# Performance work log

Measured on AMD Instinct MI355X. Metric: run time of the kernel, lower is better.

The kernel has to match this reference:

```python
import jax, jax.numpy as jnp
import numpy as np

B, T, K = 8192, 512, 12
START_TAG, STOP_TAG = 10, 11  # '[CLS]', '[SEP]' indices in default tag_map


def setup_inputs() -> dict:
    key = jax.random.key(0)
    k1, k2 = jax.random.split(key)
    logits = jax.random.normal(k1, (B, T, K), dtype=jnp.float32)
    transitions = jax.random.normal(k2, (K, K), dtype=jnp.float32)
    # constraints applied in BiLSTMCRF.__init__
    transitions = transitions.at[:, START_TAG].set(-1000.0)
    transitions = transitions.at[STOP_TAG, :].set(-1000.0)
    return {"logits": logits, "transitions": transitions}


def reference(logits, transitions):
    """Batched Viterbi decode, matching BiLSTMCRF.__viterbi_decode.

    logits: [B, T, K] emission scores (output of hidden2tag)
    transitions: [K, K] transitions[i, j] = score of tag i -> tag j
    Returns (scores [B], paths [B, T] int32).
    """
    em = jnp.swapaxes(logits, 0, 1)  # [T, B, K]

    def step(prev, emit_t):
        # prev: [B, K] trellis at t-1; v[b, i, j] = prev[b, i] + trans[i, j]
        v = prev[:, :, None] + transitions[None, :, :]  # [B, K, K]
        best = jnp.max(v, axis=1) + emit_t              # [B, K]
        bp = jnp.argmax(v, axis=1).astype(jnp.int32)    # [B, K]
        return best, bp

    final, bps = jax.lax.scan(step, em[0], em[1:])  # final: [B,K], bps: [T-1,B,K]

    scores = jnp.max(final, axis=-1)                     # [B]
    last = jnp.argmax(final, axis=-1).astype(jnp.int32)  # [B], tag at t = T-1

    def back(nxt, bp_t):
        # bp_t[b, j] = best previous tag given tag j at the next step
        cur = jnp.take_along_axis(bp_t, nxt[:, None], axis=1)[:, 0]
        return cur, cur

    # reverse scan: processes bps[T-2] .. bps[0], outputs tags for t = 0 .. T-2
    _, rest = jax.lax.scan(back, last, bps, reverse=True)  # [T-1, B]
    paths = jnp.concatenate([rest, last[None, :]], axis=0)  # [T, B]
    return scores, jnp.swapaxes(paths, 0, 1)
```

## Files before the change

kernel.cpp:

```cpp
#include <hip/hip_runtime.h>
#include <stdint.h>


namespace {

constexpr int kB = 8192;
constexpr int kT = 512;
constexpr int kK = 12;
constexpr int kRowF = 385;

typedef float vf3 __attribute__((ext_vector_type(3)));

template <int CTRL>
__device__ __forceinline__ float dppb(float x) {
    return __int_as_float(__builtin_amdgcn_update_dpp(
        0, __float_as_int(x), CTRL, 0xf, 0xf, true));
}

__global__ __launch_bounds__(64, 1) void viterbi_fused(
    const float* __restrict__ logits,
    const float* __restrict__ trans,
    float* __restrict__ out,
    uint16_t* __restrict__ bp)
{
    __shared__ float embuf[2][16][kRowF];

    const int ln    = threadIdx.x;
    const int row   = ln >> 2;
    const int c     = ln & 3;
    const int brow0 = blockIdx.x * 16;
    const int b     = brow0 + row;
    const int j0    = 3 * c;

    float TA[12], TB[12], TC[12];
#pragma unroll
    for (int i = 0; i < 12; ++i) {
        TA[i] = trans[i * kK + j0];
        TB[i] = trans[i * kK + j0 + 1];
        TC[i] = trans[i * kK + j0 + 2];
    }

    uint16_t* __restrict__ bps = bp + (size_t)b * 511 * 4 + c;

#define DMA_CHUNK(cc) do {                                                    \
    const int dsel_ = (cc) & 1;                                               \
    _Pragma("unroll")                                                         \
    for (int r_ = 0; r_ < 16; ++r_) {                                         \
        const float* gs_ = logits + (size_t)(brow0 + r_) * (kT * kK)          \
                           + (cc) * 384 + ln;                                 \
        float* ld_ = &embuf[dsel_][r_][0];                                    \
        _Pragma("unroll")                                                     \
        for (int p_ = 0; p_ < 6; ++p_) {                                      \
            __builtin_amdgcn_global_load_lds(                                 \
                (const __attribute__((address_space(1))) void*)(gs_ + p_ * 64),\
                (__attribute__((address_space(3))) void*)(ld_ + p_ * 64),     \
                4, 0, 0);                                                     \
        }                                                                     \
    }                                                                         \
} while (0)

    auto emrd = [&](int t) -> vf3 {
        const int tc = (t < kT) ? t : (kT - 1);
        return *(const vf3*)&embuf[(tc >> 5) & 1][row][(tc & 31) * 12 + j0];
    };

    DMA_CHUNK(0);
    DMA_CHUNK(1);

    __builtin_amdgcn_wave_barrier();
    __builtin_amdgcn_s_waitcnt(0x0F70);
    __builtin_amdgcn_wave_barrier();

    vf3 iv = emrd(0);
    float n0 = iv.x, n1 = iv.y, n2 = iv.z;

    vf3 e0 = emrd(1), e1 = emrd(2), e2 = emrd(3), e3 = emrd(4);
    vf3 e4 = emrd(5), e5 = emrd(6), e6 = emrd(7), e7 = emrd(8);

#define COLX(Tc, EMITc, NOUT, BIOUT) do {                                    \
    const float x0 = p0 + Tc[0],  x1 = p1 + Tc[1],  x2 = p2 + Tc[2];         \
    const float x3 = p3 + Tc[3],  x4 = p4 + Tc[4],  x5 = p5 + Tc[5];         \
    const float x6 = p6 + Tc[6],  x7 = p7 + Tc[7],  x8 = p8 + Tc[8];         \
    const float x9 = p9 + Tc[9],  x10 = p10 + Tc[10], x11 = p11 + Tc[11];    \
    const float mA = fmaxf(fmaxf(x0, x1), x2);                               \
    const float mB = fmaxf(fmaxf(x3, x4), x5);                               \
    const float mC = fmaxf(fmaxf(x6, x7), x8);                               \
    const float mD = fmaxf(fmaxf(x9, x10), x11);                             \
    const float best = fmaxf(fmaxf(mA, mB), fmaxf(mC, mD));                  \
    int bi = 11;                                                             \
    bi = (x10 == best) ? 10 : bi;  bi = (x9 == best) ? 9 : bi;               \
    bi = (x8  == best) ?  8 : bi;  bi = (x7 == best) ? 7 : bi;               \
    bi = (x6  == best) ?  6 : bi;  bi = (x5 == best) ? 5 : bi;               \
    bi = (x4  == best) ?  4 : bi;  bi = (x3 == best) ? 3 : bi;               \
    bi = (x2  == best) ?  2 : bi;  bi = (x1 == best) ? 1 : bi;               \
    bi = (x0  == best) ?  0 : bi;                                            \
    NOUT = best + (EMITc);  BIOUT = bi;                                      \
} while (0)

#define GATHER()                                                             \
    const float p0 = dppb<0x00>(n0), p1 = dppb<0x00>(n1), p2 = dppb<0x00>(n2);\
    const float p3 = dppb<0x55>(n0), p4 = dppb<0x55>(n1), p5 = dppb<0x55>(n2);\
    const float p6 = dppb<0xAA>(n0), p7 = dppb<0xAA>(n1), p8 = dppb<0xAA>(n2);\
    const float p9 = dppb<0xFF>(n0), p10 = dppb<0xFF>(n1), p11 = dppb<0xFF>(n2)

#define STEP(TT, EV) do {                                                    \
    GATHER();                                                                \
    float q0_, q1_, q2_; int b0_, b1_, b2_;                                  \
    COLX(TA, (EV).x, q0_, b0_);                                              \
    COLX(TB, (EV).y, q1_, b1_);                                              \
    COLX(TC, (EV).z, q2_, b2_);                                              \
    n0 = q0_; n1 = q1_; n2 = q2_;                                            \
    const uint32_t w_ = (uint32_t)b0_ | ((uint32_t)b1_ << 4)                 \
                        | ((uint32_t)b2_ << 8);                              \
    bps[(size_t)((TT) - 1) * 4] = (uint16_t)w_;                              \
} while (0)

    for (int n = 0; n < 63; ++n) {
        const int tb = 8 * n + 1;

        if ((n & 3) == 2) {
            __builtin_amdgcn_wave_barrier();
            __builtin_amdgcn_s_waitcnt(0x0F70);
            __builtin_amdgcn_wave_barrier();
        }
        if ((n & 3) == 3) {
            const int cc = (n >> 2) + 2;
            if (cc <= 15) {
                __builtin_amdgcn_wave_barrier();
                __builtin_amdgcn_s_waitcnt(0xC07F);
                DMA_CHUNK(cc);
                __builtin_amdgcn_wave_barrier();
            }
        }

        const vf3 f0 = emrd(tb + 8),  f1 = emrd(tb + 9);
        const vf3 f2 = emrd(tb + 10), f3 = emrd(tb + 11);
        const vf3 f4 = emrd(tb + 12), f5 = emrd(tb + 13);
        const vf3 f6 = emrd(tb + 14), f7 = emrd(tb + 15);

        STEP(tb + 0, e0); STEP(tb + 1, e1); STEP(tb + 2, e2); STEP(tb + 3, e3);
        STEP(tb + 4, e4); STEP(tb + 5, e5); STEP(tb + 6, e6); STEP(tb + 7, e7);

        e0 = f0; e1 = f1; e2 = f2; e3 = f3;
        e4 = f4; e5 = f5; e6 = f6; e7 = f7;
    }

    STEP(505, e0); STEP(506, e1); STEP(507, e2); STEP(508, e3);
    STEP(509, e4); STEP(510, e5); STEP(511, e6);

#undef STEP
#undef DMA_CHUNK

    float best;
    int last;
    {
        GATHER();
        const float mA = fmaxf(fmaxf(p0, p1), p2);
        const float mB = fmaxf(fmaxf(p3, p4), p5);
        const float mC = fmaxf(fmaxf(p6, p7), p8);
        const float mD = fmaxf(fmaxf(p9, p10), p11);
        best = fmaxf(fmaxf(mA, mB), fmaxf(mC, mD));
        int bi = 11;
        bi = (p10 == best) ? 10 : bi;  bi = (p9 == best) ? 9 : bi;
        bi = (p8  == best) ?  8 : bi;  bi = (p7 == best) ? 7 : bi;
        bi = (p6  == best) ?  6 : bi;  bi = (p5 == best) ? 5 : bi;
        bi = (p4  == best) ?  4 : bi;  bi = (p3 == best) ? 3 : bi;
        bi = (p2  == best) ?  2 : bi;  bi = (p1 == best) ? 1 : bi;
        bi = (p0  == best) ?  0 : bi;
        last = bi;
    }
#undef GATHER
#undef COLX

    __syncthreads();

    if (c == 0) {
        out[b] = best;
        float* __restrict__ paths = out + kB + (size_t)b * kT;
        paths[kT - 1] = (float)last;

        int tag = last;
        const uint2* __restrict__ rec = (const uint2*)(bp + (size_t)b * 511 * 4);
#pragma unroll 4
        for (int s = 510; s >= 0; --s) {
            const uint2 q = rec[s];
            const int d3 = (tag * 11) >> 5;
            const int rm = tag - 3 * d3;
            const uint32_t dw = (d3 & 2) ? q.y : q.x;
            const int sh = ((d3 & 1) << 4) + (rm << 2);
            tag = (int)((dw >> sh) & 0xF);
            paths[s] = (float)tag;
        }
    }
}

}

extern "C" void kernel_launch(void* const* d_in, const int* in_sizes, int n_in,
                              void* d_out, int out_size, void* d_ws, size_t ws_size,
                              hipStream_t stream) {
    const float* logits = (const float*)d_in[0];
    const float* trans  = (const float*)d_in[1];
    float* out = (float*)d_out;
    uint16_t* bp = (uint16_t*)d_ws;

    const int threads = 64;
    const int blocks = kB / 16;
    viterbi_fused<<<blocks, threads, 0, stream>>>(logits, trans, out, bp);
}
```

Baseline: 496.0 us.

## Map one lane per tag with 4 rows per wave and packed backpointers

```diff
diff --git a/kernel.cpp b/kernel.cpp
--- a/kernel.cpp
+++ b/kernel.cpp
@@ -7,45 +7,43 @@
 constexpr int kB = 8192;
 constexpr int kT = 512;
 constexpr int kK = 12;
-constexpr int kRowF = 385;
-
-typedef float vf3 __attribute__((ext_vector_type(3)));
-
-template <int CTRL>
-__device__ __forceinline__ float dppb(float x) {
-    return __int_as_float(__builtin_amdgcn_update_dpp(
-        0, __float_as_int(x), CTRL, 0xf, 0xf, true));
-}
-
-__global__ __launch_bounds__(64, 1) void viterbi_fused(
+constexpr int kRows = 4;
+constexpr int kRowF = 392;
+
+template <int I>
+__device__ __forceinline__ float bcast16(float x) {
+    return __int_as_float(__builtin_amdgcn_ds_swizzle(
+        __float_as_int(x), (I << 5) | 0x10));
+}
+
+__global__ __launch_bounds__(64, 2) void viterbi_fused(
     const float* __restrict__ logits,
     const float* __restrict__ trans,
     float* __restrict__ out,
-    uint16_t* __restrict__ bp)
+    uint32_t* __restrict__ bp)
 {
-    __shared__ float embuf[2][16][kRowF];
+    __shared__ float embuf[2][kRows][kRowF];
 
     const int ln    = threadIdx.x;
-    const int row   = ln >> 2;
-    const int c     = ln & 3;
-    const int brow0 = blockIdx.x * 16;
-    const int b     = brow0 + row;
-    const int j0    = 3 * c;
-
-    float TA[12], TB[12], TC[12];
-#pragma unroll
-    for (int i = 0; i < 12; ++i) {
-        TA[i] = trans[i * kK + j0];
-        TB[i] = trans[i * kK + j0 + 1];
-        TC[i] = trans[i * kK + j0 + 2];
-    }
-
-    uint16_t* __restrict__ bps = bp + (size_t)b * 511 * 4 + c;
+    const int grp   = ln >> 4;
+    const int jl    = ln & 15;
+    const int j     = (jl < 12) ? jl : 11;
+    const int brow0 = blockIdx.x * kRows;
+    const int b     = brow0 + grp;
+
+    const float T0 = trans[0 * kK + j],  T1 = trans[1 * kK + j];
+    const float T2 = trans[2 * kK + j],  T3 = trans[3 * kK + j];
+    const float T4 = trans[4 * kK + j],  T5 = trans[5 * kK + j];
+    const float T6 = trans[6 * kK + j],  T7 = trans[7 * kK + j];
+    const float T8 = trans[8 * kK + j],  T9 = trans[9 * kK + j];
+    const float T10 = trans[10 * kK + j], T11 = trans[11 * kK + j];
+
+    uint32_t* __restrict__ bpq = bp + (size_t)b * 1024 + jl;
 
 #define DMA_CHUNK(cc) do {                                                    \
     const int dsel_ = (cc) & 1;                                               \
     _Pragma("unroll")                                                         \
-    for (int r_ = 0; r_ < 16; ++r_) {                                         \
+    for (int r_ = 0; r_ < kRows; ++r_) {                                      \
         const float* gs_ = logits + (size_t)(brow0 + r_) * (kT * kK)          \
                            + (cc) * 384 + ln;                                 \
         float* ld_ = &embuf[dsel_][r_][0];                                    \
@@ -59,9 +57,9 @@
     }                                                                         \
 } while (0)
 
-    auto emrd = [&](int t) -> vf3 {
+    auto emrd = [&](int t) -> float {
         const int tc = (t < kT) ? t : (kT - 1);
-        return *(const vf3*)&embuf[(tc >> 5) & 1][row][(tc & 31) * 12 + j0];
+        return embuf[(tc >> 5) & 1][grp][(tc & 31) * 12 + jl];
     };
 
     DMA_CHUNK(0);
@@ -71,60 +69,51 @@
     __builtin_amdgcn_s_waitcnt(0x0F70);
     __builtin_amdgcn_wave_barrier();
 
-    vf3 iv = emrd(0);
-    float n0 = iv.x, n1 = iv.y, n2 = iv.z;
-
-    vf3 e0 = emrd(1), e1 = emrd(2), e2 = emrd(3), e3 = emrd(4);
-    vf3 e4 = emrd(5), e5 = emrd(6), e6 = emrd(7), e7 = emrd(8);
-
-#define COLX(Tc, EMITc, NOUT, BIOUT) do {                                    \
-    const float x0 = p0 + Tc[0],  x1 = p1 + Tc[1],  x2 = p2 + Tc[2];         \
-    const float x3 = p3 + Tc[3],  x4 = p4 + Tc[4],  x5 = p5 + Tc[5];         \
-    const float x6 = p6 + Tc[6],  x7 = p7 + Tc[7],  x8 = p8 + Tc[8];         \
-    const float x9 = p9 + Tc[9],  x10 = p10 + Tc[10], x11 = p11 + Tc[11];    \
-    const float mA = fmaxf(fmaxf(x0, x1), x2);                               \
-    const float mB = fmaxf(fmaxf(x3, x4), x5);                               \
-    const float mC = fmaxf(fmaxf(x6, x7), x8);                               \
-    const float mD = fmaxf(fmaxf(x9, x10), x11);                             \
-    const float best = fmaxf(fmaxf(mA, mB), fmaxf(mC, mD));                  \
-    int bi = 11;                                                             \
-    bi = (x10 == best) ? 10 : bi;  bi = (x9 == best) ? 9 : bi;               \
-    bi = (x8  == best) ?  8 : bi;  bi = (x7 == best) ? 7 : bi;               \
-    bi = (x6  == best) ?  6 : bi;  bi = (x5 == best) ? 5 : bi;               \
-    bi = (x4  == best) ?  4 : bi;  bi = (x3 == best) ? 3 : bi;               \
-    bi = (x2  == best) ?  2 : bi;  bi = (x1 == best) ? 1 : bi;               \
-    bi = (x0  == best) ?  0 : bi;                                            \
-    NOUT = best + (EMITc);  BIOUT = bi;                                      \
+    float nv = emrd(0);
+    uint32_t acc = 0u;
+
+    float e0 = emrd(1), e1 = emrd(2), e2 = emrd(3), e3 = emrd(4);
+    float e4 = emrd(5), e5 = emrd(6), e6 = emrd(7), e7 = emrd(8);
+
+#define STEP(TT, EV) do {                                                     \
+    const float p0 = bcast16<0>(nv),  p1 = bcast16<1>(nv);                    \
+    const float p2 = bcast16<2>(nv),  p3 = bcast16<3>(nv);                    \
+    const float p4 = bcast16<4>(nv),  p5 = bcast16<5>(nv);                    \
+    const float p6 = bcast16<6>(nv),  p7 = bcast16<7>(nv);                    \
+    const float p8 = bcast16<8>(nv),  p9 = bcast16<9>(nv);                    \
+    const float p10 = bcast16<10>(nv), p11 = bcast16<11>(nv);                 \
+    const float x0 = p0 + T0,  x1 = p1 + T1,  x2 = p2 + T2;                   \
+    const float x3 = p3 + T3,  x4 = p4 + T4,  x5 = p5 + T5;                   \
+    const float x6 = p6 + T6,  x7 = p7 + T7,  x8 = p8 + T8;                   \
+    const float x9 = p9 + T9,  x10 = p10 + T10, x11 = p11 + T11;              \
+    const float mA = fmaxf(fmaxf(x0, x1), x2);                                \
+    const float mB = fmaxf(fmaxf(x3, x4), x5);                                \
+    const float mC = fmaxf(fmaxf(x6, x7), x8);                                \
+    const float mD = fmaxf(fmaxf(x9, x10), x11);                              \
+    const float best = fmaxf(fmaxf(mA, mB), fmaxf(mC, mD));                   \
+    int gA = (x1 == mA) ? 1 : 2;    gA = (x0 == mA) ? 0 : gA;                 \
+    int gB = (x4 == mB) ? 4 : 5;    gB = (x3 == mB) ? 3 : gB;                 \
+    int gC = (x7 == mC) ? 7 : 8;    gC = (x6 == mC) ? 6 : gC;                 \
+    int gD = (x10 == mD) ? 10 : 11; gD = (x9 == mD) ? 9 : gD;                 \
+    int bi = gD;                                                              \
+    bi = (mC == best) ? gC : bi;                                              \
+    bi = (mB == best) ? gB : bi;                                              \
+    bi = (mA == best) ? gA : bi;                                              \
+    nv = best + (EV);                                                         \
+    acc |= (uint32_t)bi << (4 * (((TT) - 1) & 7));                            \
 } while (0)
 
-#define GATHER()                                                             \
-    const float p0 = dppb<0x00>(n0), p1 = dppb<0x00>(n1), p2 = dppb<0x00>(n2);\
-    const float p3 = dppb<0x55>(n0), p4 = dppb<0x55>(n1), p5 = dppb<0x55>(n2);\
-    const float p6 = dppb<0xAA>(n0), p7 = dppb<0xAA>(n1), p8 = dppb<0xAA>(n2);\
-    const float p9 = dppb<0xFF>(n0), p10 = dppb<0xFF>(n1), p11 = dppb<0xFF>(n2)
-
-#define STEP(TT, EV) do {                                                    \
-    GATHER();                                                                \
-    float q0_, q1_, q2_; int b0_, b1_, b2_;                                  \
-    COLX(TA, (EV).x, q0_, b0_);                                              \
-    COLX(TB, (EV).y, q1_, b1_);                                              \
-    COLX(TC, (EV).z, q2_, b2_);                                              \
-    n0 = q0_; n1 = q1_; n2 = q2_;                                            \
-    const uint32_t w_ = (uint32_t)b0_ | ((uint32_t)b1_ << 4)                 \
-                        | ((uint32_t)b2_ << 8);                              \
-    bps[(size_t)((TT) - 1) * 4] = (uint16_t)w_;                              \
-} while (0)
-
-    for (int n = 0; n < 63; ++n) {
-        const int tb = 8 * n + 1;
-
-        if ((n & 3) == 2) {
+#pragma unroll 1
+    for (int sb = 0; sb < 63; ++sb) {
+        const int tb = 8 * sb + 1;
+
+        if ((sb & 3) == 2) {
             __builtin_amdgcn_wave_barrier();
             __builtin_amdgcn_s_waitcnt(0x0F70);
             __builtin_amdgcn_wave_barrier();
         }
-        if ((n & 3) == 3) {
-            const int cc = (n >> 2) + 2;
+        if ((sb & 3) == 3) {
+            const int cc = (sb >> 2) + 2;
             if (cc <= 15) {
                 __builtin_amdgcn_wave_barrier();
                 __builtin_amdgcn_s_waitcnt(0xC07F);
@@ -133,13 +122,16 @@
             }
         }
 
-        const vf3 f0 = emrd(tb + 8),  f1 = emrd(tb + 9);
-        const vf3 f2 = emrd(tb + 10), f3 = emrd(tb + 11);
-        const vf3 f4 = emrd(tb + 12), f5 = emrd(tb + 13);
-        const vf3 f6 = emrd(tb + 14), f7 = emrd(tb + 15);
+        const float f0 = emrd(tb + 8),  f1 = emrd(tb + 9);
+        const float f2 = emrd(tb + 10), f3 = emrd(tb + 11);
+        const float f4 = emrd(tb + 12), f5 = emrd(tb + 13);
+        const float f6 = emrd(tb + 14), f7 = emrd(tb + 15);
 
         STEP(tb + 0, e0); STEP(tb + 1, e1); STEP(tb + 2, e2); STEP(tb + 3, e3);
         STEP(tb + 4, e4); STEP(tb + 5, e5); STEP(tb + 6, e6); STEP(tb + 7, e7);
+
+        bpq[sb * 16] = acc;
+        acc = 0u;
 
         e0 = f0; e1 = f1; e2 = f2; e3 = f3;
         e4 = f4; e5 = f5; e6 = f6; e7 = f7;
@@ -147,6 +139,7 @@
 
     STEP(505, e0); STEP(506, e1); STEP(507, e2); STEP(508, e3);
     STEP(509, e4); STEP(510, e5); STEP(511, e6);
+    bpq[63 * 16] = acc;
 
 #undef STEP
 #undef DMA_CHUNK
@@ -154,44 +147,74 @@
     float best;
     int last;
     {
-        GATHER();
+        const float p0 = bcast16<0>(nv),  p1 = bcast16<1>(nv);
+        const float p2 = bcast16<2>(nv),  p3 = bcast16<3>(nv);
+        const float p4 = bcast16<4>(nv),  p5 = bcast16<5>(nv);
+        const float p6 = bcast16<6>(nv),  p7 = bcast16<7>(nv);
+        const float p8 = bcast16<8>(nv),  p9 = bcast16<9>(nv);
+        const float p10 = bcast16<10>(nv), p11 = bcast16<11>(nv);
         const float mA = fmaxf(fmaxf(p0, p1), p2);
         const float mB = fmaxf(fmaxf(p3, p4), p5);
         const float mC = fmaxf(fmaxf(p6, p7), p8);
         const float mD = fmaxf(fmaxf(p9, p10), p11);
         best = fmaxf(fmaxf(mA, mB), fmaxf(mC, mD));
-        int bi = 11;
-        bi = (p10 == best) ? 10 : bi;  bi = (p9 == best) ? 9 : bi;
-        bi = (p8  == best) ?  8 : bi;  bi = (p7 == best) ? 7 : bi;
-        bi = (p6  == best) ?  6 : bi;  bi = (p5 == best) ? 5 : bi;
-        bi = (p4  == best) ?  4 : bi;  bi = (p3 == best) ? 3 : bi;
-        bi = (p2  == best) ?  2 : bi;  bi = (p1 == best) ? 1 : bi;
-        bi = (p0  == best) ?  0 : bi;
+        int gA = (p1 == mA) ? 1 : 2;    gA = (p0 == mA) ? 0 : gA;
+        int gB = (p4 == mB) ? 4 : 5;    gB = (p3 == mB) ? 3 : gB;
+        int gC = (p7 == mC) ? 7 : 8;    gC = (p6 == mC) ? 6 : gC;
+        int gD = (p10 == mD) ? 10 : 11; gD = (p9 == mD) ? 9 : gD;
+        int bi = gD;
+        bi = (mC == best) ? gC : bi;
+        bi = (mB == best) ? gB : bi;
+        bi = (mA == best) ? gA : bi;
         last = bi;
     }
-#undef GATHER
-#undef COLX
 
     __syncthreads();
 
-    if (c == 0) {
+#define BTS(SUB, PB) do {                                                     \
+    const uint32_t e0_ = (tag & 1) ? qa.y : qa.x;                             \
+    const uint32_t e1_ = (tag & 1) ? qa.w : qa.z;                             \
+    const uint32_t e2_ = (tag & 1) ? qb.y : qb.x;                             \
+    const uint32_t e3_ = (tag & 1) ? qb.w : qb.z;                             \
+    const uint32_t e4_ = (tag & 1) ? qc.y : qc.x;                             \
+    const uint32_t e5_ = (tag & 1) ? qc.w : qc.z;                             \
+    const uint32_t f0_ = (tag & 2) ? e1_ : e0_;                               \
+    const uint32_t f1_ = (tag & 2) ? e3_ : e2_;                               \
+    const uint32_t f2_ = (tag & 2) ? e5_ : e4_;                               \
+    const uint32_t g0_ = (tag & 4) ? f1_ : f0_;                               \
+    const uint32_t dw_ = (tag >= 8) ? f2_ : g0_;                              \
+    tag = (int)((dw_ >> (4 * (SUB))) & 0xFu);                                 \
+    paths[(PB) + (SUB)] = (float)tag;                                         \
+} while (0)
+
+    if (jl == 0) {
         out[b] = best;
         float* __restrict__ paths = out + kB + (size_t)b * kT;
         paths[kT - 1] = (float)last;
 
         int tag = last;
-        const uint2* __restrict__ rec = (const uint2*)(bp + (size_t)b * 511 * 4);
-#pragma unroll 4
-        for (int s = 510; s >= 0; --s) {
-            const uint2 q = rec[s];
-            const int d3 = (tag * 11) >> 5;
-            const int rm = tag - 3 * d3;
-            const uint32_t dw = (d3 & 2) ? q.y : q.x;
-            const int sh = ((d3 & 1) << 4) + (rm << 2);
-            tag = (int)((dw >> sh) & 0xF);
-            paths[s] = (float)tag;
+        const uint4* __restrict__ rec = (const uint4*)(bp + (size_t)b * 1024);
+
+        uint4 qa = rec[63 * 4 + 0], qb = rec[63 * 4 + 1], qc = rec[63 * 4 + 2];
+        uint4 na = rec[62 * 4 + 0], nb = rec[62 * 4 + 1], nc = rec[62 * 4 + 2];
+
+        BTS(6, 504); BTS(5, 504); BTS(4, 504); BTS(3, 504);
+        BTS(2, 504); BTS(1, 504); BTS(0, 504);
+
+#pragma unroll 1
+        for (int blk = 62; blk >= 0; --blk) {
+            qa = na; qb = nb; qc = nc;
+            if (blk > 0) {
+                na = rec[blk * 4 - 4];
+                nb = rec[blk * 4 - 3];
+                nc = rec[blk * 4 - 2];
+            }
+            const int pb = blk * 8;
+            BTS(7, pb); BTS(6, pb); BTS(5, pb); BTS(4, pb);
+            BTS(3, pb); BTS(2, pb); BTS(1, pb); BTS(0, pb);
         }
     }
+#undef BTS
 }
 
 }
@@ -202,9 +225,9 @@
     const float* logits = (const float*)d_in[0];
     const float* trans  = (const float*)d_in[1];
     float* out = (float*)d_out;
-    uint16_t* bp = (uint16_t*)d_ws;
+    uint32_t* bp = (uint32_t*)d_ws;
 
     const int threads = 64;
-    const int blocks = kB / 16;
+    const int blocks = kB / kRows;
     viterbi_fused<<<blocks, threads, 0, stream>>>(logits, trans, out, bp);
 }
```

Result: no change. 491.6 us (-0.9%).

## Replace LDS DMA staging with direct per-lane global emission loads

Applied to the files above, without the earlier changes.

```diff
diff --git a/kernel.cpp b/kernel.cpp
--- a/kernel.cpp
+++ b/kernel.cpp
@@ -7,7 +7,6 @@
 constexpr int kB = 8192;
 constexpr int kT = 512;
 constexpr int kK = 12;
-constexpr int kRowF = 385;
 
 typedef float vf3 __attribute__((ext_vector_type(3)));
 
@@ -17,20 +16,17 @@
         0, __float_as_int(x), CTRL, 0xf, 0xf, true));
 }
 
-__global__ __launch_bounds__(64, 1) void viterbi_fused(
+__global__ __launch_bounds__(64) void viterbi_fused(
     const float* __restrict__ logits,
     const float* __restrict__ trans,
     float* __restrict__ out,
     uint16_t* __restrict__ bp)
 {
-    __shared__ float embuf[2][16][kRowF];
-
-    const int ln    = threadIdx.x;
-    const int row   = ln >> 2;
-    const int c     = ln & 3;
-    const int brow0 = blockIdx.x * 16;
-    const int b     = brow0 + row;
-    const int j0    = 3 * c;
+    const int ln = threadIdx.x;
+    const int qd = ln >> 2;
+    const int c  = ln & 3;
+    const int b  = blockIdx.x * 16 + qd;
+    const int j0 = 3 * c;
 
     float TA[12], TB[12], TC[12];
 #pragma unroll
@@ -42,40 +38,26 @@
 
     uint16_t* __restrict__ bps = bp + (size_t)b * 511 * 4 + c;
 
-#define DMA_CHUNK(cc) do {                                                    \
-    const int dsel_ = (cc) & 1;                                               \
-    _Pragma("unroll")                                                         \
-    for (int r_ = 0; r_ < 16; ++r_) {                                         \
-        const float* gs_ = logits + (size_t)(brow0 + r_) * (kT * kK)          \
-                           + (cc) * 384 + ln;                                 \
-        float* ld_ = &embuf[dsel_][r_][0];                                    \
-        _Pragma("unroll")                                                     \
-        for (int p_ = 0; p_ < 6; ++p_) {                                      \
-            __builtin_amdgcn_global_load_lds(                                 \
-                (const __attribute__((address_space(1))) void*)(gs_ + p_ * 64),\
-                (__attribute__((address_space(3))) void*)(ld_ + p_ * 64),     \
-                4, 0, 0);                                                     \
-        }                                                                     \
-    }                                                                         \
-} while (0)
+    const float* __restrict__ gem = logits + (size_t)b * (kT * kK) + j0;
 
-    auto emrd = [&](int t) -> vf3 {
+    auto ld = [&](int t) -> vf3 {
         const int tc = (t < kT) ? t : (kT - 1);
-        return *(const vf3*)&embuf[(tc >> 5) & 1][row][(tc & 31) * 12 + j0];
+        vf3 v;
+        __builtin_memcpy(&v, gem + (size_t)tc * kK, 12);
+        return v;
     };
 
-    DMA_CHUNK(0);
-    DMA_CHUNK(1);
-
-    __builtin_amdgcn_wave_barrier();
-    __builtin_amdgcn_s_waitcnt(0x0F70);
-    __builtin_amdgcn_wave_barrier();
-
-    vf3 iv = emrd(0);
+    vf3 iv = ld(0);
     float n0 = iv.x, n1 = iv.y, n2 = iv.z;
 
-    vf3 e0 = emrd(1), e1 = emrd(2), e2 = emrd(3), e3 = emrd(4);
-    vf3 e4 = emrd(5), e5 = emrd(6), e6 = emrd(7), e7 = emrd(8);
+    vf3 e0 = ld(1), e1 = ld(2), e2 = ld(3), e3 = ld(4);
+    vf3 e4 = ld(5), e5 = ld(6), e6 = ld(7), e7 = ld(8);
+
+#define GATHER()                                                             \
+    const float p0 = dppb<0x00>(n0), p1 = dppb<0x00>(n1), p2 = dppb<0x00>(n2);\
+    const float p3 = dppb<0x55>(n0), p4 = dppb<0x55>(n1), p5 = dppb<0x55>(n2);\
+    const float p6 = dppb<0xAA>(n0), p7 = dppb<0xAA>(n1), p8 = dppb<0xAA>(n2);\
+    const float p9 = dppb<0xFF>(n0), p10 = dppb<0xFF>(n1), p11 = dppb<0xFF>(n2)
 
 #define COLX(Tc, EMITc, NOUT, BIOUT) do {                                    \
     const float x0 = p0 + Tc[0],  x1 = p1 + Tc[1],  x2 = p2 + Tc[2];         \
@@ -97,12 +79,6 @@
     NOUT = best + (EMITc);  BIOUT = bi;                                      \
 } while (0)
 
-#define GATHER()                                                             \
-    const float p0 = dppb<0x00>(n0), p1 = dppb<0x00>(n1), p2 = dppb<0x00>(n2);\
-    const float p3 = dppb<0x55>(n0), p4 = dppb<0x55>(n1), p5 = dppb<0x55>(n2);\
-    const float p6 = dppb<0xAA>(n0), p7 = dppb<0xAA>(n1), p8 = dppb<0xAA>(n2);\
-    const float p9 = dppb<0xFF>(n0), p10 = dppb<0xFF>(n1), p11 = dppb<0xFF>(n2)
-
 #define STEP(TT, EV) do {                                                    \
     GATHER();                                                                \
     float q0_, q1_, q2_; int b0_, b1_, b2_;                                  \
@@ -115,28 +91,14 @@
     bps[(size_t)((TT) - 1) * 4] = (uint16_t)w_;                              \
 } while (0)
 
-    for (int n = 0; n < 63; ++n) {
-        const int tb = 8 * n + 1;
+#pragma unroll 1
+    for (int sb = 0; sb < 63; ++sb) {
+        const int tb = 8 * sb + 1;
 
-        if ((n & 3) == 2) {
-            __builtin_amdgcn_wave_barrier();
-            __builtin_amdgcn_s_waitcnt(0x0F70);
-            __builtin_amdgcn_wave_barrier();
-        }
-        if ((n & 3) == 3) {
-            const int cc = (n >> 2) + 2;
-            if (cc <= 15) {
-                __builtin_amdgcn_wave_barrier();
-                __builtin_amdgcn_s_waitcnt(0xC07F);
-                DMA_CHUNK(cc);
-                __builtin_amdgcn_wave_barrier();
-            }
-        }
-
-        const vf3 f0 = emrd(tb + 8),  f1 = emrd(tb + 9);
-        const vf3 f2 = emrd(tb + 10), f3 = emrd(tb + 11);
-        const vf3 f4 = emrd(tb + 12), f5 = emrd(tb + 13);
-        const vf3 f6 = emrd(tb + 14), f7 = emrd(tb + 15);
+        const vf3 f0 = ld(tb + 8),  f1 = ld(tb + 9);
+        const vf3 f2 = ld(tb + 10), f3 = ld(tb + 11);
+        const vf3 f4 = ld(tb + 12), f5 = ld(tb + 13);
+        const vf3 f6 = ld(tb + 14), f7 = ld(tb + 15);
 
         STEP(tb + 0, e0); STEP(tb + 1, e1); STEP(tb + 2, e2); STEP(tb + 3, e3);
         STEP(tb + 4, e4); STEP(tb + 5, e5); STEP(tb + 6, e6); STEP(tb + 7, e7);
@@ -149,7 +111,6 @@
     STEP(509, e4); STEP(510, e5); STEP(511, e6);
 
 #undef STEP
-#undef DMA_CHUNK
 
     float best;
     int last;
```

Result: faster. 429.7 us (-13.4%).
